# Optimization experiments

Hardware: AMD Instinct MI355X
Metric: run time of the kernel (lower is better)

## Reference

```python
import jax, jax.numpy as jnp
import numpy as np

N_NODES = 20000
N_EDGES = 320000
N_FEATS = 256
DIM_H = 64
HEADS = 8
N_CLASSES = 16
NEG_SLOPE = 0.2  # PyG GATv2Conv default negative_slope


def _glorot(key, shape):
    fan_in, fan_out = shape[0], shape[-1]
    lim = jnp.sqrt(6.0 / (fan_in + fan_out))
    return jax.random.uniform(key, shape, jnp.float32, -lim, lim)


def setup_inputs() -> dict:
    key = jax.random.key(0)
    ks = jax.random.split(key, 12)
    x = jax.random.normal(ks[0], (N_NODES, N_FEATS), jnp.float32)
    edge_index = jax.random.randint(ks[1], (2, N_EDGES), 0, N_NODES, jnp.int64)
    # layer 1: in=256 -> heads=8, out=64 (concat -> 512)
    W_l1 = _glorot(ks[2], (N_FEATS, HEADS * DIM_H))
    b_l1 = jnp.zeros((HEADS * DIM_H,), jnp.float32)
    W_r1 = _glorot(ks[3], (N_FEATS, HEADS * DIM_H))
    b_r1 = jnp.zeros((HEADS * DIM_H,), jnp.float32)
    att1 = _glorot(ks[4], (HEADS, DIM_H))
    bias1 = jnp.zeros((HEADS * DIM_H,), jnp.float32)
    # layer 2: in=512 -> heads=1, out=16
    W_l2 = _glorot(ks[5], (HEADS * DIM_H, N_CLASSES))
    b_l2 = jnp.zeros((N_CLASSES,), jnp.float32)
    W_r2 = _glorot(ks[6], (HEADS * DIM_H, N_CLASSES))
    b_r2 = jnp.zeros((N_CLASSES,), jnp.float32)
    att2 = _glorot(ks[7], (1, N_CLASSES))
    bias2 = jnp.zeros((N_CLASSES,), jnp.float32)
    return dict(x=x, edge_index=edge_index,
                W_l1=W_l1, b_l1=b_l1, W_r1=W_r1, b_r1=b_r1, att1=att1, bias1=bias1,
                W_l2=W_l2, b_l2=b_l2, W_r2=W_r2, b_r2=b_r2, att2=att2, bias2=bias2)


def gatv2_conv(x, src, dst, W_l, b_l, W_r, b_r, att, bias, n_nodes):
    """GATv2Conv (PyG defaults: share_weights=False, concat=True, no dropout in eval).
    src/dst already include self-loops. att: [H, D]."""
    H, D = att.shape
    x_l = (x @ W_l + b_l).reshape(n_nodes, H, D)  # source transform
    x_r = (x @ W_r + b_r).reshape(n_nodes, H, D)  # target transform
    # per-edge message: [E, H, D]
    m = jax.nn.leaky_relu(x_l[src] + x_r[dst], NEG_SLOPE)
    e = jnp.einsum('ehd,hd->eh', m, att)  # [E, H] attention logits
    # segment softmax over incoming edges of each dst node
    e_max = jax.ops.segment_max(e, dst, num_segments=n_nodes)  # [N, H]
    p = jnp.exp(e - e_max[dst])
    denom = jax.ops.segment_sum(p, dst, num_segments=n_nodes)  # [N, H]
    alpha = p / denom[dst]  # [E, H]
    out = jax.ops.segment_sum(alpha[:, :, None] * x_l[src], dst, num_segments=n_nodes)
    return out.reshape(n_nodes, H * D) + bias


def reference(x, edge_index, W_l1, b_l1, W_r1, b_r1, att1, bias1,
              W_l2, b_l2, W_r2, b_r2, att2, bias2):
    n = x.shape[0]
    loop = jnp.arange(n, dtype=edge_index.dtype)  # add_self_loops=True
    src = jnp.concatenate([edge_index[0], loop])
    dst = jnp.concatenate([edge_index[1], loop])
    h = gatv2_conv(x, src, dst, W_l1, b_l1, W_r1, b_r1, att1, bias1, n)
    h = jax.nn.relu(h)
    out = gatv2_conv(h, src, dst, W_l2, b_l2, W_r2, b_r2, att2, bias2, n)
    return out
```

## Files before the change

### kernel.cpp

```cpp
#include <hip/hip_runtime.h>
#include <hip/hip_bf16.h>
#include <stdint.h>

#define N_NODES 20000
#define MPAD    20096
#define N_EDG   320000
#define ET      (N_EDG + N_NODES)
#define NFE     256
#define HD      512
#define NH      8
#define DH      64
#define NC      16

typedef __attribute__((ext_vector_type(8))) short short8;
typedef __attribute__((ext_vector_type(8))) _Float16 half8;
typedef __attribute__((ext_vector_type(4))) float f32x4;

#define AS1 __attribute__((address_space(1)))
#define AS3 __attribute__((address_space(3)))

__device__ __forceinline__ unsigned short f2bf(float f) {
    unsigned u = __float_as_uint(f);
    return (unsigned short)((u + 0x7FFFu + ((u >> 16) & 1u)) >> 16);
}
__device__ __forceinline__ float bf2f(unsigned short s) {
    return __uint_as_float(((unsigned)s) << 16);
}

__global__ void count_deg(const int* __restrict__ ei, int* __restrict__ deg) {
    int e = blockIdx.x * 256 + threadIdx.x;
    if (e >= ET) return;
    int dst = (e < N_EDG) ? ei[N_EDG + e] : (e - N_EDG);
    atomicAdd(&deg[dst], 1);
}

__global__ __launch_bounds__(1024) void scan_offsets(const int* __restrict__ deg,
                                                     int* __restrict__ offs,
                                                     int* __restrict__ cur) {
    __shared__ int wsum[16];
    __shared__ int carry_s;
    int t = threadIdx.x;
    int wid = t >> 6, lane = t & 63;
    if (t == 0) { carry_s = 0; offs[0] = 0; }
    __syncthreads();
    for (int base = 0; base < N_NODES; base += 1024) {
        int i = base + t;
        int v = (i < N_NODES) ? deg[i] : 0;
        int sv = v;
        #pragma unroll
        for (int off = 1; off < 64; off <<= 1) {
            int n = __shfl_up(sv, off);
            if (lane >= off) sv += n;
        }
        if (lane == 63) wsum[wid] = sv;
        __syncthreads();
        int wpre = 0;
        #pragma unroll
        for (int w = 0; w < 16; ++w) wpre += (w < wid) ? wsum[w] : 0;
        int incl = sv + wpre + carry_s;
        if (i < N_NODES) {
            offs[i + 1] = incl;
            cur[i] = incl - v;
        }
        __syncthreads();
        if (t == 1023) carry_s = incl;
        __syncthreads();
    }
}

__global__ void fill_csr(const int* __restrict__ ei, int* __restrict__ cur,
                         int* __restrict__ esrc) {
    int e = blockIdx.x * 256 + threadIdx.x;
    if (e >= ET) return;
    int src, dst;
    if (e < N_EDG) { src = ei[e]; dst = ei[N_EDG + e]; }
    else { src = e - N_EDG; dst = src; }
    int pos = atomicAdd(&cur[dst], 1);
    esrc[pos] = src;
}

__global__ __launch_bounds__(256) void split_x(const float* __restrict__ x,
        unsigned short* __restrict__ xh, unsigned short* __restrict__ xl) {
    int i = (blockIdx.x * 256 + threadIdx.x) * 4;
    if (i >= N_NODES * NFE) return;
    float4 v = *reinterpret_cast<const float4*>(x + i);
    ushort4 h, l;
    h.x = f2bf(v.x); l.x = f2bf(v.x - bf2f(h.x));
    h.y = f2bf(v.y); l.y = f2bf(v.y - bf2f(h.y));
    h.z = f2bf(v.z); l.z = f2bf(v.z - bf2f(h.z));
    h.w = f2bf(v.w); l.w = f2bf(v.w - bf2f(h.w));
    *reinterpret_cast<ushort4*>(xh + i) = h;
    *reinterpret_cast<ushort4*>(xl + i) = l;
}

__global__ __launch_bounds__(256) void split_w(const float* __restrict__ Wl,
        const float* __restrict__ Wr, unsigned short* __restrict__ Wth,
        unsigned short* __restrict__ Wtl) {
    const float* W = blockIdx.y ? Wr : Wl;
    unsigned short* oh = Wth + (size_t)blockIdx.y * (HD * NFE);
    unsigned short* ol = Wtl + (size_t)blockIdx.y * (HD * NFE);
    int i = blockIdx.x * 256 + threadIdx.x;
    if (i >= NFE * HD) return;
    int k = i >> 9, n = i & 511;
    float v = W[i];
    unsigned short h = f2bf(v), l = f2bf(v - bf2f(h));
    oh[n * NFE + k] = h;
    ol[n * NFE + k] = l;
}

#define ROWP 157
#define G1_NWG (8 * ROWP * 2)
__global__ __launch_bounds__(256) void gemm1m(
        const unsigned short* __restrict__ xh, const unsigned short* __restrict__ xl,
        const unsigned short* __restrict__ Wth, const unsigned short* __restrict__ Wtl,
        const float* __restrict__ bl, const float* __restrict__ br,
        _Float16* __restrict__ outl, _Float16* __restrict__ outr) {
    __shared__ short Ah[4 * 128 * 8], Al[4 * 128 * 8];
    __shared__ short Bh[4 * 64 * 8],  Blo[4 * 64 * 8];

    int flat = blockIdx.x;
    int wgid = (flat & 7) * (G1_NWG / 8) + (flat >> 3);
    int z = wgid / (8 * ROWP);
    int rem = wgid - z * (8 * ROWP);
    int rowp = rem >> 3, colb = rem & 7;
    int row0 = rowp * 128, col0 = colb * 64;

    const unsigned short* Wh = Wth + (size_t)z * (HD * NFE);
    const unsigned short* Wl_ = Wtl + (size_t)z * (HD * NFE);
    const float* bias = z ? br : bl;
    _Float16* out = z ? outr : outl;

    int tid = threadIdx.x;
    int w = tid >> 6, lane = tid & 63;
    int wr0 = (w >> 1) * 64, wn0 = (w & 1) * 32;

    const unsigned short* asrc = (w & 1) ? xl : xh;
    short* adst = (w & 1) ? Al : Ah;
    int tb = (w >> 1) * 4;
    const unsigned short* bsrc = (w < 2) ? Wh : Wl_;
    short* bdst = (w < 2) ? Bh : Blo;
    int btb = (w & 1) * 2;

    f32x4 acc[4][2] = {};
    int kb_l = lane >> 4, r16 = lane & 15;

    for (int k0 = 0; k0 < NFE; k0 += 32) {
        #pragma unroll
        for (int t = 0; t < 4; ++t) {
            int tt = tb + t;
            int kb = tt >> 1, rr = (tt & 1) * 64 + lane;
            const unsigned short* g = asrc + (size_t)(row0 + rr) * NFE + k0 + kb * 8;
            __builtin_amdgcn_global_load_lds((const AS1 void*)g,
                                             (AS3 void*)(adst + tt * 512), 16, 0, 0);
        }
        #pragma unroll
        for (int t = 0; t < 2; ++t) {
            int tt = btb + t;
            const unsigned short* g = bsrc + (size_t)(col0 + lane) * NFE + k0 + tt * 8;
            __builtin_amdgcn_global_load_lds((const AS1 void*)g,
                                             (AS3 void*)(bdst + tt * 512), 16, 0, 0);
        }
        __syncthreads();

        short8 ah[4], al[4], bh[2], blv[2];
        #pragma unroll
        for (int mi = 0; mi < 4; ++mi) {
            int idx = (kb_l * 128 + wr0 + mi * 16 + r16) * 8;
            ah[mi] = *reinterpret_cast<const short8*>(&Ah[idx]);
            al[mi] = *reinterpret_cast<const short8*>(&Al[idx]);
        }
        #pragma unroll
        for (int ni = 0; ni < 2; ++ni) {
            int idx = (kb_l * 64 + wn0 + ni * 16 + r16) * 8;
            bh[ni]  = *reinterpret_cast<const short8*>(&Bh[idx]);
            blv[ni] = *reinterpret_cast<const short8*>(&Blo[idx]);
        }
        #pragma unroll
        for (int mi = 0; mi < 4; ++mi)
            #pragma unroll
            for (int ni = 0; ni < 2; ++ni) {
                acc[mi][ni] = __builtin_amdgcn_mfma_f32_16x16x32_bf16(ah[mi], bh[ni],  acc[mi][ni], 0, 0, 0);
                acc[mi][ni] = __builtin_amdgcn_mfma_f32_16x16x32_bf16(ah[mi], blv[ni], acc[mi][ni], 0, 0, 0);
                acc[mi][ni] = __builtin_amdgcn_mfma_f32_16x16x32_bf16(al[mi], bh[ni],  acc[mi][ni], 0, 0, 0);
            }
        __syncthreads();
    }

    int orow_base = row0 + wr0 + (lane >> 4) * 4;
    int ocol_base = col0 + wn0 + r16;
    #pragma unroll
    for (int mi = 0; mi < 4; ++mi)
        #pragma unroll
        for (int ni = 0; ni < 2; ++ni) {
            int col = ocol_base + ni * 16;
            float bv = bias[col];
            #pragma unroll
            for (int r = 0; r < 4; ++r) {
                int row = orow_base + mi * 16 + r;
                if (row < N_NODES)
                    out[(size_t)row * HD + col] = (_Float16)(acc[mi][ni][r] + bv);
            }
        }
}

__global__ __launch_bounds__(256) void fused1(const int* __restrict__ offs,
        const int* __restrict__ esrc,
        const _Float16* __restrict__ xl1, const _Float16* __restrict__ xr1,
        const float* __restrict__ att1, const float* __restrict__ bias1,
        float* __restrict__ hout) {
    int wid = (blockIdx.x * 256 + threadIdx.x) >> 6;
    int lane = threadIdx.x & 63;
    if (wid >= N_NODES) return;
    int beg = offs[wid], end = offs[wid + 1];

    float att[8], xr[8];
    *reinterpret_cast<float4*>(&att[0]) = *reinterpret_cast<const float4*>(att1 + lane * 8);
    *reinterpret_cast<float4*>(&att[4]) = *reinterpret_cast<const float4*>(att1 + lane * 8 + 4);
    {
        half8 hv = *reinterpret_cast<const half8*>(xr1 + (size_t)wid * HD + lane * 8);
        #pragma unroll
        for (int q = 0; q < 8; ++q) xr[q] = (float)hv[q];
    }

    float m = -3.4e38f, s = 0.f;
    float acc[8] = {};

    half8 xsp;
    xsp = *reinterpret_cast<const half8*>(xl1 + (size_t)esrc[beg] * HD + lane * 8);

    for (int j = beg; j < end; ++j) {
        half8 curh = xsp;
        if (j + 1 < end)
            xsp = *reinterpret_cast<const half8*>(xl1 + (size_t)esrc[j + 1] * HD + lane * 8);
        float cx[8];
        #pragma unroll
        for (int q = 0; q < 8; ++q) cx[q] = (float)curh[q];

        float v = 0.f;
        #pragma unroll
        for (int q = 0; q < 8; ++q) {
            float t = cx[q] + xr[q];
            t = t > 0.f ? t : 0.2f * t;
            v = fmaf(t, att[q], v);
        }
        v += __shfl_xor(v, 1);
        v += __shfl_xor(v, 2);
        v += __shfl_xor(v, 4);
        float nm = fmaxf(m, v);
        float sc = __expf(m - nm);
        float p  = __expf(v - nm);
        s = s * sc + p;
        #pragma unroll
        for (int q = 0; q < 8; ++q) acc[q] = fmaf(acc[q], sc, p * cx[q]);
        m = nm;
    }

    float inv = 1.0f / s;
    float o[8];
    #pragma unroll
    for (int q = 0; q < 8; ++q) {
        float bi = bias1[lane * 8 + q];
        o[q] = fmaxf(fmaf(acc[q], inv, bi), 0.f);
    }
    float* op = hout + (size_t)wid * HD + lane * 8;
    *reinterpret_cast<float4*>(op)     = *reinterpret_cast<float4*>(&o[0]);
    *reinterpret_cast<float4*>(op + 4) = *reinterpret_cast<float4*>(&o[4]);
}

__global__ __launch_bounds__(256) void gemm2(const float* __restrict__ h,
        const float* __restrict__ Wl2, const float* __restrict__ bl2,
        const float* __restrict__ Wr2, const float* __restrict__ br2,
        float* __restrict__ xl2, float* __restrict__ xr2) {
    int tx = threadIdx.x % 32;
    int ty = threadIdx.x / 32;
    int row = blockIdx.x * 8 + ty;
    if (row >= N_NODES) return;
    const float* W = (tx < 16) ? Wl2 : Wr2;
    int c = tx & 15;
    const float4* hr4 = reinterpret_cast<const float4*>(h + (size_t)row * HD);
    float acc = 0.f;
    #pragma unroll 4
    for (int k4 = 0; k4 < HD / 4; ++k4) {
        float4 v = hr4[k4];
        int k = k4 * 4;
        acc = fmaf(v.x, W[(k + 0) * NC + c], acc);
        acc = fmaf(v.y, W[(k + 1) * NC + c], acc);
        acc = fmaf(v.z, W[(k + 2) * NC + c], acc);
        acc = fmaf(v.w, W[(k + 3) * NC + c], acc);
    }
    if (tx < 16) xl2[(size_t)row * NC + c] = acc + bl2[c];
    else         xr2[(size_t)row * NC + c] = acc + br2[c];
}

__global__ __launch_bounds__(256) void fused2(const int* __restrict__ offs,
        const int* __restrict__ esrc,
        const float* __restrict__ xl2, const float* __restrict__ xr2,
        const float* __restrict__ att2, const float* __restrict__ bias2,
        float* __restrict__ out) {
    int wid = (blockIdx.x * 256 + threadIdx.x) >> 6;
    int lane = threadIdx.x & 63;
    if (wid >= N_NODES) return;
    int g = lane >> 4, d = lane & 15;
    int beg = offs[wid], end = offs[wid + 1];

    float xr = xr2[(size_t)wid * NC + d];
    float at = att2[d];
    float m = -3.4e38f, s = 0.f, acc = 0.f;

    for (int j = beg + g; j < end; j += 4) {
        int src = esrc[j];
        float xs = xl2[(size_t)src * NC + d];
        float t = xs + xr;
        t = t > 0.f ? t : 0.2f * t;
        float v = t * at;
        v += __shfl_xor(v, 1);
        v += __shfl_xor(v, 2);
        v += __shfl_xor(v, 4);
        v += __shfl_xor(v, 8);
        float nm = fmaxf(m, v);
        float sc = __expf(m - nm), p = __expf(v - nm);
        s = s * sc + p;
        acc = fmaf(acc, sc, p * xs);
        m = nm;
    }
    #pragma unroll
    for (int off = 16; off < 64; off <<= 1) {
        float om = __shfl_xor(m, off);
        float os = __shfl_xor(s, off);
        float oa = __shfl_xor(acc, off);
        float nm = fmaxf(m, om);
        float c1 = __expf(m - nm), c2 = __expf(om - nm);
        s = s * c1 + os * c2;
        acc = acc * c1 + oa * c2;
        m = nm;
    }
    if (lane < 16) out[(size_t)wid * NC + d] = acc / s + bias2[d];
}

extern "C" void kernel_launch(void* const* d_in, const int* in_sizes, int n_in,
                              void* d_out, int out_size, void* d_ws, size_t ws_size,
                              hipStream_t stream) {
    const float* x     = (const float*)d_in[0];
    const int*   ei    = (const int*)d_in[1];
    const float* W_l1  = (const float*)d_in[2];
    const float* b_l1  = (const float*)d_in[3];
    const float* W_r1  = (const float*)d_in[4];
    const float* b_r1  = (const float*)d_in[5];
    const float* att1  = (const float*)d_in[6];
    const float* bias1 = (const float*)d_in[7];
    const float* W_l2  = (const float*)d_in[8];
    const float* b_l2  = (const float*)d_in[9];
    const float* W_r2  = (const float*)d_in[10];
    const float* b_r2  = (const float*)d_in[11];
    const float* att2  = (const float*)d_in[12];
    const float* bias2 = (const float*)d_in[13];
    float* out = (float*)d_out;

    char* ws = (char*)d_ws;
    _Float16* xl1 = (_Float16*)ws; ws += (size_t)N_NODES * HD * sizeof(_Float16);
    _Float16* xr1 = (_Float16*)ws; ws += (size_t)N_NODES * HD * sizeof(_Float16);
    float* hbuf = (float*)ws; ws += (size_t)N_NODES * HD * sizeof(float);
    float* xl2  = (float*)ws; ws += (size_t)N_NODES * NC * sizeof(float);
    float* xr2  = (float*)ws; ws += (size_t)N_NODES * NC * sizeof(float);
    int* deg    = (int*)ws; ws += (size_t)N_NODES * sizeof(int);
    int* offs   = (int*)ws; ws += (size_t)(N_NODES + 1) * sizeof(int);
    int* cursor = (int*)ws; ws += (size_t)N_NODES * sizeof(int);
    int* esrc   = (int*)ws; ws += (size_t)ET * sizeof(int);
    unsigned short* xh  = (unsigned short*)ws; ws += (size_t)MPAD * NFE * sizeof(short);
    unsigned short* xlo = (unsigned short*)ws; ws += (size_t)MPAD * NFE * sizeof(short);
    unsigned short* Wth = (unsigned short*)ws; ws += (size_t)2 * HD * NFE * sizeof(short);
    unsigned short* Wtl = (unsigned short*)ws; ws += (size_t)2 * HD * NFE * sizeof(short);

    hipMemsetAsync(deg, 0, N_NODES * sizeof(int), stream);
    count_deg<<<(ET + 255) / 256, 256, 0, stream>>>(ei, deg);
    scan_offsets<<<1, 1024, 0, stream>>>(deg, offs, cursor);
    fill_csr<<<(ET + 255) / 256, 256, 0, stream>>>(ei, cursor, esrc);

    split_x<<<(N_NODES * NFE / 4 + 255) / 256, 256, 0, stream>>>(x, xh, xlo);
    split_w<<<dim3((NFE * HD + 255) / 256, 2), 256, 0, stream>>>(W_l1, W_r1, Wth, Wtl);

    gemm1m<<<G1_NWG, 256, 0, stream>>>(xh, xlo, Wth, Wtl, b_l1, b_r1, xl1, xr1);
    fused1<<<(N_NODES + 3) / 4, 256, 0, stream>>>(offs, esrc, xl1, xr1, att1, bias1, hbuf);

    gemm2<<<(N_NODES + 7) / 8, 256, 0, stream>>>(hbuf, W_l2, b_l2, W_r2, b_r2, xl2, xr2);
    fused2<<<(N_NODES + 3) / 4, 256, 0, stream>>>(offs, esrc, xl2, xr2, att2, bias2, out);
}
```

Before: 389.3 us.

## Double-buffer LDS staging in split-bf16 GEMM and switch to row-major tile layout

The layer-1 GEMM now keeps two LDS buffers and issues the global-to-LDS loads for the next K-slice before computing on the current one, so memory latency can overlap with the MFMA work. The staging layout also changes to row-major 32-wide rows, with each lane loading a 16-byte K chunk, which gives more contiguous global reads. The cost is doubled LDS use, which may lower occupancy. The row-major layout can also cause LDS bank conflicts on the short8 fragment reads, since the row stride is 64 bytes.

```diff
diff --git a/kernel.cpp b/kernel.cpp
--- a/kernel.cpp
+++ b/kernel.cpp
@@ -115,8 +115,8 @@
         const unsigned short* __restrict__ Wth, const unsigned short* __restrict__ Wtl,
         const float* __restrict__ bl, const float* __restrict__ br,
         _Float16* __restrict__ outl, _Float16* __restrict__ outr) {
-    __shared__ short Ah[4 * 128 * 8], Al[4 * 128 * 8];
-    __shared__ short Bh[4 * 64 * 8],  Blo[4 * 64 * 8];
+    __shared__ __align__(16) short Ah[2][128 * 32], Al[2][128 * 32];
+    __shared__ __align__(16) short Bh[2][64 * 32],  Bls[2][64 * 32];
 
     int flat = blockIdx.x;
     int wgid = (flat & 7) * (G1_NWG / 8) + (flat >> 3);
@@ -125,7 +125,7 @@
     int rowp = rem >> 3, colb = rem & 7;
     int row0 = rowp * 128, col0 = colb * 64;
 
-    const unsigned short* Wh = Wth + (size_t)z * (HD * NFE);
+    const unsigned short* Wh  = Wth + (size_t)z * (HD * NFE);
     const unsigned short* Wl_ = Wtl + (size_t)z * (HD * NFE);
     const float* bias = z ? br : bl;
     _Float16* out = z ? outr : outl;
@@ -133,60 +133,62 @@
     int tid = threadIdx.x;
     int w = tid >> 6, lane = tid & 63;
     int wr0 = (w >> 1) * 64, wn0 = (w & 1) * 32;
-
-    const unsigned short* asrc = (w & 1) ? xl : xh;
-    short* adst = (w & 1) ? Al : Ah;
-    int tb = (w >> 1) * 4;
-    const unsigned short* bsrc = (w < 2) ? Wh : Wl_;
-    short* bdst = (w < 2) ? Bh : Blo;
-    int btb = (w & 1) * 2;
+    int r16 = lane & 15, kb_l = lane >> 4;
+    int rsub = lane >> 2, kch = lane & 3;
 
     f32x4 acc[4][2] = {};
-    int kb_l = lane >> 4, r16 = lane & 15;
-
-    for (int k0 = 0; k0 < NFE; k0 += 32) {
-        #pragma unroll
-        for (int t = 0; t < 4; ++t) {
-            int tt = tb + t;
-            int kb = tt >> 1, rr = (tt & 1) * 64 + lane;
-            const unsigned short* g = asrc + (size_t)(row0 + rr) * NFE + k0 + kb * 8;
-            __builtin_amdgcn_global_load_lds((const AS1 void*)g,
-                                             (AS3 void*)(adst + tt * 512), 16, 0, 0);
-        }
-        #pragma unroll
-        for (int t = 0; t < 2; ++t) {
-            int tt = btb + t;
-            const unsigned short* g = bsrc + (size_t)(col0 + lane) * NFE + k0 + tt * 8;
-            __builtin_amdgcn_global_load_lds((const AS1 void*)g,
-                                             (AS3 void*)(bdst + tt * 512), 16, 0, 0);
-        }
-        __syncthreads();
-
-        short8 ah[4], al[4], bh[2], blv[2];
+
+    auto stage = [&](int buf, int k0) {
+        #pragma unroll
+        for (int i = 0; i < 2; ++i) {
+            int inst = 2 * w + i;
+            int rl = inst * 16 + rsub;
+            size_t goff = (size_t)(row0 + rl) * NFE + k0 + kch * 8;
+            __builtin_amdgcn_global_load_lds((const AS1 void*)(xh + goff),
+                                             (AS3 void*)(&Ah[buf][inst * 512]), 16, 0, 0);
+            __builtin_amdgcn_global_load_lds((const AS1 void*)(xl + goff),
+                                             (AS3 void*)(&Al[buf][inst * 512]), 16, 0, 0);
+        }
+        int cl = w * 16 + rsub;
+        size_t boff = (size_t)(col0 + cl) * NFE + k0 + kch * 8;
+        __builtin_amdgcn_global_load_lds((const AS1 void*)(Wh + boff),
+                                         (AS3 void*)(&Bh[buf][w * 512]), 16, 0, 0);
+        __builtin_amdgcn_global_load_lds((const AS1 void*)(Wl_ + boff),
+                                         (AS3 void*)(&Bls[buf][w * 512]), 16, 0, 0);
+    };
+
+    stage(0, 0);
+    __syncthreads();
+
+    for (int t = 0; t < 8; ++t) {
+        int buf = t & 1;
+        if (t < 7) stage(buf ^ 1, (t + 1) * 32);
+
+        short8 ah[4], alv[4], bhv[2], blv[2];
         #pragma unroll
         for (int mi = 0; mi < 4; ++mi) {
-            int idx = (kb_l * 128 + wr0 + mi * 16 + r16) * 8;
-            ah[mi] = *reinterpret_cast<const short8*>(&Ah[idx]);
-            al[mi] = *reinterpret_cast<const short8*>(&Al[idx]);
+            int idx = (wr0 + mi * 16 + r16) * 32 + kb_l * 8;
+            ah[mi]  = *reinterpret_cast<const short8*>(&Ah[buf][idx]);
+            alv[mi] = *reinterpret_cast<const short8*>(&Al[buf][idx]);
         }
         #pragma unroll
         for (int ni = 0; ni < 2; ++ni) {
-            int idx = (kb_l * 64 + wn0 + ni * 16 + r16) * 8;
-            bh[ni]  = *reinterpret_cast<const short8*>(&Bh[idx]);
-            blv[ni] = *reinterpret_cast<const short8*>(&Blo[idx]);
+            int idx = (wn0 + ni * 16 + r16) * 32 + kb_l * 8;
+            bhv[ni] = *reinterpret_cast<const short8*>(&Bh[buf][idx]);
+            blv[ni] = *reinterpret_cast<const short8*>(&Bls[buf][idx]);
         }
         #pragma unroll
         for (int mi = 0; mi < 4; ++mi)
             #pragma unroll
             for (int ni = 0; ni < 2; ++ni) {
-                acc[mi][ni] = __builtin_amdgcn_mfma_f32_16x16x32_bf16(ah[mi], bh[ni],  acc[mi][ni], 0, 0, 0);
-                acc[mi][ni] = __builtin_amdgcn_mfma_f32_16x16x32_bf16(ah[mi], blv[ni], acc[mi][ni], 0, 0, 0);
-                acc[mi][ni] = __builtin_amdgcn_mfma_f32_16x16x32_bf16(al[mi], bh[ni],  acc[mi][ni], 0, 0, 0);
+                acc[mi][ni] = __builtin_amdgcn_mfma_f32_16x16x32_bf16(ah[mi],  bhv[ni], acc[mi][ni], 0, 0, 0);
+                acc[mi][ni] = __builtin_amdgcn_mfma_f32_16x16x32_bf16(ah[mi],  blv[ni], acc[mi][ni], 0, 0, 0);
+                acc[mi][ni] = __builtin_amdgcn_mfma_f32_16x16x32_bf16(alv[mi], bhv[ni], acc[mi][ni], 0, 0, 0);
             }
         __syncthreads();
     }
 
-    int orow_base = row0 + wr0 + (lane >> 4) * 4;
+    int orow_base = row0 + wr0 + kb_l * 4;
     int ocol_base = col0 + wn0 + r16;
     #pragma unroll
     for (int mi = 0; mi < 4; ++mi)
```

After: 366.2 us. 5.9% less time.
